# Kernel tuning notes

Measured on AMD Instinct MI355X. Metric: run time of the kernel, lower is better.

## Reference

```python
import jax, jax.numpy as jnp
import numpy as np

D_MODEL = 2048
N_HEADS = 16
N_KV = 4
D_HEAD = 128
D1 = 64
D2 = 64
WSIZE = 1024
EPS = 1e-6
ROPE_BASE = 10000.0


def _rmsnorm(x):
    # RMSNorm over last dim, no affine weight
    return x * jax.lax.rsqrt(jnp.mean(x * x, axis=-1, keepdims=True) + EPS)


def _apply_rope(x, cos, sin):
    # x: (..., D2); cos/sin: (1, T, 1, D2//2)
    h = D2 // 2
    x1, x2 = x[..., :h], x[..., h:]
    return jnp.concatenate([x1 * cos + x2 * sin, -x1 * sin + x2 * cos], axis=-1)


def setup_inputs() -> dict:
    key = jax.random.key(0)
    ks = jax.random.split(key, 6)
    B, T = 2, 2048
    return {
        "hidden_states": jax.random.normal(ks[0], (B, T, D_MODEL), dtype=jnp.float32),
        "W_qkv": jax.random.normal(ks[1], (D_MODEL, (N_HEADS + N_KV) * D_HEAD), dtype=jnp.float32) * 0.02,
        "W_rk": jax.random.normal(ks[2], (D_MODEL, D2), dtype=jnp.float32) * 0.02,
        "b_rk": jax.random.normal(ks[3], (D2,), dtype=jnp.float32) * 0.02,
        "softmax_scaler": jnp.ones((N_HEADS,), dtype=jnp.float32),
        "W_g": jax.random.normal(ks[5], (D_MODEL, D_MODEL), dtype=jnp.float32) * 0.02,
    }


def reference(hidden_states, W_qkv, W_rk, b_rk, softmax_scaler, W_g):
    x = hidden_states
    B, T, _ = x.shape
    # fused qkv projection + per-(head,token) RMSNorm (qk_norm)
    qkv = (x @ W_qkv).reshape(B, T, N_HEADS + N_KV, D_HEAD)
    qkv = _rmsnorm(qkv)
    q, kv = qkv[:, :, :N_HEADS], qkv[:, :, N_HEADS:]
    q_nope, q_rope = q[..., :D1], q[..., D1:]

    # head-tied rope key: shared across all heads
    k_rope = (x @ W_rk + b_rk)[:, :, None, :]  # (B, T, 1, D2)

    # rotary embedding (start_pos = 0)
    inv_freq = 1.0 / (ROPE_BASE ** (jnp.arange(0, D2, 2, dtype=jnp.float32) / D2))
    freqs = jnp.arange(T, dtype=jnp.float32)[:, None] * inv_freq[None, :]  # (T, D2//2)
    cos = jnp.cos(freqs)[None, :, None, :]
    sin = jnp.sin(freqs)[None, :, None, :]
    q_rope = _apply_rope(q_rope, cos, sin)
    k_rope = jnp.broadcast_to(_apply_rope(k_rope, cos, sin), (B, T, N_HEADS, D2))

    q = jnp.concatenate([q_nope, q_rope], axis=-1)  # (B, T, H, D_HEAD)

    # scalable softmax: scale q by per-head scaler * log(min(pos, wsize))
    pos = jnp.arange(1, T + 1, dtype=jnp.float32)
    log_pos = jnp.log(jnp.minimum(pos, float(WSIZE)))[None, :, None, None]
    q = softmax_scaler[None, None, :, None] * log_pos * q

    # tied k/v: first D1 of kv shared between k and v; repeat kv heads (GQA)
    kv_tied, v = kv[..., :D1], kv[..., D1:]
    rep = N_HEADS // N_KV
    kv_tied = jnp.repeat(kv_tied, rep, axis=2)  # (B, T, H, D1)
    v = jnp.repeat(v, rep, axis=2)              # (B, T, H, D2)
    k = jnp.concatenate([kv_tied, k_rope], axis=-1)   # (B, T, H, D_HEAD)
    v_full = jnp.concatenate([kv_tied, v], axis=-1)   # (B, T, H, D_HEAD)

    # sliding-window causal attention: key j valid iff i - WSIZE <= j <= i
    scores = jnp.einsum('bthd,bshd->bhts', q, k) / np.float32(np.sqrt(D_HEAD))
    i = jnp.arange(T)[:, None]
    j = jnp.arange(T)[None, :]
    mask = (j <= i) & (j >= i - WSIZE)
    scores = jnp.where(mask[None, None], scores, jnp.float32(-1e30))
    p = jax.nn.softmax(scores, axis=-1)
    y = jnp.einsum('bhts,bshd->bthd', p, v_full)  # (B, T, H, D_HEAD)

    # elementwise silu gate
    g = (x @ W_g).reshape(B, T, N_HEADS, D_HEAD)
    return y * jax.nn.silu(g)
```

## Files before the change

kernel.cpp:

```cpp
#include <hip/hip_runtime.h>

typedef _Float16 f16;
typedef _Float16 half8 __attribute__((ext_vector_type(8)));
typedef _Float16 half4_t __attribute__((ext_vector_type(4)));
typedef float f32x4 __attribute__((ext_vector_type(4)));

#define T_SEQ 2048
#define B_SZ 2
#define DM 2048
#define NH 16
#define NKV 4
#define DH 128
#define NQKV 2560
#define NALL 4736
#define NALLP 4864
#define COL_RK 2560
#define COL_G 2688
#define M_ROWS 4096
#define WIN 1024

typedef __attribute__((address_space(1))) const unsigned int guint;
typedef __attribute__((address_space(3))) unsigned int luint;
__device__ __forceinline__ void gload16(const void* g, void* l) {
  __builtin_amdgcn_global_load_lds((guint*)g, (luint*)l, 16, 0, 0);
}

__global__ void k_cvt(const float* __restrict__ in, f16* __restrict__ out, int n) {
  int i = (blockIdx.x * 256 + threadIdx.x) * 4;
  if (i >= n) return;
  float4 v = *(const float4*)(in + i);
  half4_t o;
  o[0] = (f16)v.x; o[1] = (f16)v.y; o[2] = (f16)v.z; o[3] = (f16)v.w;
  *(half4_t*)(out + i) = o;
}

__global__ __launch_bounds__(256) void k_cvt_t(const float* __restrict__ W,
                                               f16* __restrict__ Wt, int K, int N) {
  __shared__ float tile[32][33];
  int k0 = blockIdx.x * 32, n0 = blockIdx.y * 32;
  int tx = threadIdx.x & 31, ty = threadIdx.x >> 5;
#pragma unroll
  for (int r = 0; r < 32; r += 8)
    tile[ty + r][tx] = W[(size_t)(k0 + ty + r) * N + n0 + tx];
  __syncthreads();
#pragma unroll
  for (int r = 0; r < 32; r += 8)
    Wt[(size_t)(n0 + ty + r) * K + k0 + tx] = (f16)tile[tx][ty + r];
}

__global__ __launch_bounds__(256) void k_vt(const f16* __restrict__ v, f16* __restrict__ vt) {
  __shared__ f16 tile[32][34];
  int t0 = blockIdx.x * 32, d0 = blockIdx.y * 32, m = blockIdx.z;
  int tx = threadIdx.x & 31, ty = threadIdx.x >> 5;
  const f16* src = v + (size_t)m * T_SEQ * DH;
  f16* dst = vt + (size_t)m * T_SEQ * DH;
#pragma unroll
  for (int r = 0; r < 32; r += 8)
    tile[ty + r][tx] = src[(size_t)(t0 + ty + r) * DH + d0 + tx];
  __syncthreads();
#pragma unroll
  for (int r = 0; r < 32; r += 8)
    dst[(size_t)(d0 + ty + r) * T_SEQ + t0 + tx] = tile[tx][ty + r];
}

#define GEMM_PHASE(cb, kk, sb, koff)                                                        \
  {                                                                                         \
    char* Ab = lds + (cb) * 32768 + (kk) * 16384;                                           \
    char* Bb = lds + 65536 + (cb) * 16384 + (kk) * 8192;                                    \
    half8 af[4], bf[4];                                                                     \
    _Pragma("unroll")                                                                       \
    for (int i = 0; i < 4; ++i)                                                             \
      af[i] = *(const half8*)(Ab + (wm * 64 + i * 16 + fr) * 64 + xsl);                     \
    _Pragma("unroll")                                                                       \
    for (int j = 0; j < 4; ++j)                                                             \
      bf[j] = *(const half8*)(Bb + (wn * 64 + j * 16 + fr) * 64 + xsl);                     \
    gload16(Ag0 + (koff) + (kk) * 32, lds + (sb) * 32768 + (kk) * 16384 + w * 1024);        \
    gload16(Ag1 + (koff) + (kk) * 32, lds + (sb) * 32768 + (kk) * 16384 + 8192 + w * 1024); \
    gload16(Bg + (koff) + (kk) * 32, lds + 65536 + (sb) * 16384 + (kk) * 8192 + w * 1024);  \
    __builtin_amdgcn_s_barrier();                                                           \
    __builtin_amdgcn_sched_barrier(0);                                                      \
    asm volatile("s_waitcnt lgkmcnt(0)" ::: "memory");                                      \
    __builtin_amdgcn_sched_barrier(0);                                                      \
    __builtin_amdgcn_s_setprio(1);                                                          \
    _Pragma("unroll")                                                                       \
    for (int i = 0; i < 4; ++i)                                                             \
      _Pragma("unroll")                                                                     \
      for (int j = 0; j < 4; ++j)                                                           \
        acc[i][j] = __builtin_amdgcn_mfma_f32_16x16x32_f16(af[i], bf[j], acc[i][j], 0, 0, 0); \
    __builtin_amdgcn_s_setprio(0);                                                          \
    asm volatile("s_waitcnt vmcnt(3)" ::: "memory");                                        \
    __builtin_amdgcn_s_barrier();                                                           \
    __builtin_amdgcn_sched_barrier(0);                                                      \
  }

__global__ __launch_bounds__(512, 2) void k_gemm8(const f16* __restrict__ A,
                                                  const f16* __restrict__ Bt,
                                                  f16* __restrict__ C) {
  __shared__ __align__(16) char lds[98304];
  const int K = DM;
  unsigned orig = blockIdx.y * 38u + blockIdx.x;
  unsigned swz = (orig & 7u) * 76u + (orig >> 3);
  int m0 = (int)(swz / 38u) * 256;
  int n0 = (int)(swz % 38u) * 128;
  int tid = threadIdx.x, lane = tid & 63, w = tid >> 6;
  int wm = w >> 1, wn = w & 1;
  int fr = lane & 15, fq = lane >> 4;
  int xsl = (fq ^ ((fr >> 1) & 3)) << 4;
  int sr = tid >> 2, ss = tid & 3;
  int scol = (ss ^ ((sr >> 1) & 3)) * 8;
  f32x4 acc[4][4] = {};
  const f16* Ag0 = A + (size_t)(m0 + sr) * K + scol;
  const f16* Ag1 = A + (size_t)(m0 + 128 + sr) * K + scol;
  const f16* Bg  = Bt + (size_t)(n0 + sr) * K + scol;

  gload16(Ag0, lds + w * 1024);
  gload16(Ag1, lds + 8192 + w * 1024);
  gload16(Bg, lds + 65536 + w * 1024);
  gload16(Ag0 + 32, lds + 16384 + w * 1024);
  gload16(Ag1 + 32, lds + 16384 + 8192 + w * 1024);
  gload16(Bg + 32, lds + 65536 + 8192 + w * 1024);
  asm volatile("s_waitcnt vmcnt(3)" ::: "memory");
  __builtin_amdgcn_s_barrier();
  __builtin_amdgcn_sched_barrier(0);

  for (int kt = 0; kt < 32; ++kt) {
    int cb = kt & 1;
    int nt = kt < 31 ? kt + 1 : 31;
    int sb = nt & 1;
    int koff = nt * 64;
    GEMM_PHASE(cb, 0, sb, koff);
    GEMM_PHASE(cb, 1, sb, koff);
  }

#pragma unroll
  for (int i = 0; i < 4; ++i) {
    int row = m0 + wm * 64 + i * 16 + fq * 4;
#pragma unroll
    for (int j = 0; j < 4; ++j) {
      int col = n0 + wn * 64 + j * 16 + fr;
      f16* Cp = C + (size_t)row * NALLP + col;
#pragma unroll
      for (int rr = 0; rr < 4; ++rr) Cp[(size_t)rr * NALLP] = (f16)acc[i][j][rr];
    }
  }
}

__global__ __launch_bounds__(256) void k_postproc(
    const f16* __restrict__ CA,
    const float* __restrict__ brk, const float* __restrict__ sscal,
    f16* __restrict__ q16, f16* __restrict__ k16, f16* __restrict__ v16) {
  int row = blockIdx.x;
  int b = row >> 11, t = row & 2047;
  int lane = threadIdx.x & 63, wid = threadIdx.x >> 6;
  int ridx = lane & 31;
  float inv_freq = powf(10000.0f, -(float)(2 * ridx) / 64.0f);
  float fr = (float)t * inv_freq;
  float cs = cosf(fr), sn = sinf(fr);
  float logpos = logf(fminf((float)(t + 1), 1024.0f));
  const float rsqrt_d_log2e = 0.08838834764831845f * 1.4426950408889634f;
  const f16* Crow = CA + (size_t)row * NALLP;
#pragma unroll
  for (int p = 0; p < 5; ++p) {
    int h = p * 4 + wid;
    float v0 = (float)Crow[h * 128 + lane];
    float v1 = (float)Crow[h * 128 + 64 + lane];
    float ss = v0 * v0 + v1 * v1;
#pragma unroll
    for (int m = 1; m < 64; m <<= 1) ss += __shfl_xor(ss, m);
    float rms = rsqrtf(ss * (1.0f / 128.0f) + 1e-6f);
    v0 *= rms; v1 *= rms;
    if (h < NH) {
      float part = __shfl_xor(v1, 32);
      float vr = (lane < 32) ? (v1 * cs + part * sn) : (v1 * cs - part * sn);
      float scale = sscal[h] * logpos * rsqrt_d_log2e;
      size_t qb = ((size_t)(b * NH + h) * T_SEQ + t) * DH;
      q16[qb + lane]      = (f16)(v0 * scale);
      q16[qb + 64 + lane] = (f16)(vr * scale);
    } else {
      int hk = h - NH;
      size_t kb = ((size_t)(b * NKV + hk) * T_SEQ + t) * DH;
      k16[kb + lane]      = (f16)v0;
      v16[kb + lane]      = (f16)v0;
      v16[kb + 64 + lane] = (f16)v1;
    }
  }
  if (wid == 0) {
    float kr = (float)Crow[COL_RK + lane] + brk[lane];
    float part = __shfl_xor(kr, 32);
    float vr = (lane < 32) ? (kr * cs + part * sn) : (kr * cs - part * sn);
    f16 hv = (f16)vr;
#pragma unroll
    for (int hk = 0; hk < NKV; ++hk)
      k16[((size_t)(b * NKV + hk) * T_SEQ + t) * DH + 64 + lane] = hv;
  }
}

__global__ __launch_bounds__(512, 2) void k_attn(
    const f16* __restrict__ q16, const f16* __restrict__ k16, const f16* __restrict__ vt16,
    const f16* __restrict__ gA, float* __restrict__ out) {
  __shared__ __align__(16) f16 Ks[64 * DH];
  __shared__ __align__(16) f16 Vs[DH * 64];
  __shared__ __align__(16) f16 Ps[8 * 16 * 64];
  int bx = blockIdx.x;
  int qt = (bx & 1) ? (15 - (bx >> 1)) : (bx >> 1);
  int h = blockIdx.y, b = blockIdx.z, hk = h >> 2;
  int tid = threadIdx.x, lane = tid & 63, w = tid >> 6;
  int i0 = qt * 128, iw = i0 + w * 16;
  int fr = lane & 15, fq = lane >> 4;

  char* Ksb = (char*)Ks;
  char* Vsb = (char*)Vs;
  char* Psb = (char*)Ps + w * 2048;

  const f16* qbase = q16 + ((size_t)(b * NH + h) * T_SEQ + iw + fr) * DH;
  half8 qf[4];
#pragma unroll
  for (int kb = 0; kb < 4; ++kb) qf[kb] = *(const half8*)&qbase[kb * 32 + fq * 8];

  f32x4 o[8] = {};
  float mrow[4] = {-1e30f, -1e30f, -1e30f, -1e30f};
  float lrow[4] = {0.f, 0.f, 0.f, 0.f};

  const f16* kg = k16 + (size_t)(b * NKV + hk) * T_SEQ * DH;
  const f16* vg = vt16 + (size_t)(b * NKV + hk) * T_SEQ * DH;

  int jtTop = qt * 2 + 1;
  int jt0 = qt >= 8 ? qt * 2 - 16 : 0;
  for (int jt = jt0; jt <= jtTop; ++jt) {
    int j0 = jt * 64;
#pragma unroll
    for (int i = 0; i < 2; ++i) {
      int r = i * 32 + (tid >> 4);
      int c = (tid & 15) ^ (r & 7);
      gload16(kg + (size_t)(j0 + r) * DH + c * 8, Ksb + i * 8192 + w * 1024);
    }
#pragma unroll
    for (int i = 0; i < 2; ++i) {
      int r = i * 64 + (tid >> 3);
      int c = (tid & 7) ^ (r & 7);
      gload16(vg + (size_t)r * T_SEQ + j0 + c * 8, Vsb + i * 8192 + w * 1024);
    }
    __syncthreads();

    bool active = (jt == jtTop) ? (w >= 4)
                : ((qt >= 8 && jt == jt0) ? (w < 4) : true);
    if (active) {
      f32x4 s[4] = {};
      __builtin_amdgcn_s_setprio(1);
#pragma unroll
      for (int nf = 0; nf < 4; ++nf) {
        int row = nf * 16 + fr;
        int sw = fr & 7;
#pragma unroll
        for (int kb = 0; kb < 4; ++kb) {
          half8 bfv = *(const half8*)(Ksb + row * 256 + ((((kb << 2) | fq) ^ sw) << 4));
          s[nf] = __builtin_amdgcn_mfma_f32_16x16x32_f16(qf[kb], bfv, s[nf], 0, 0, 0);
        }
      }
      __builtin_amdgcn_s_setprio(0);
      int il = (w << 4) + (fq << 2);
      if (jt >= (qt << 1)) {
        int dc = (jt << 6) - i0;
#pragma unroll
        for (int nf = 0; nf < 4; ++nf) {
          int jo = nf * 16 + fr + dc;
#pragma unroll
          for (int r = 0; r < 4; ++r)
            if (jo > il + r) s[nf][r] = -3e38f;
        }
      } else if (qt >= 8 && jt - jt0 < 2) {
        int dl = (jt - jt0) << 6;
#pragma unroll
        for (int nf = 0; nf < 4; ++nf) {
          int jo = nf * 16 + fr + dl;
#pragma unroll
          for (int r = 0; r < 4; ++r)
            if (jo < il + r) s[nf][r] = -3e38f;
        }
      }
      float tm[4];
#pragma unroll
      for (int r = 0; r < 4; ++r)
        tm[r] = fmaxf(fmaxf(s[0][r], s[1][r]), fmaxf(s[2][r], s[3][r]));
#pragma unroll
      for (int r = 0; r < 4; ++r) {
        tm[r] = fmaxf(tm[r], __shfl_xor(tm[r], 1));
        tm[r] = fmaxf(tm[r], __shfl_xor(tm[r], 2));
        tm[r] = fmaxf(tm[r], __shfl_xor(tm[r], 4));
        tm[r] = fmaxf(tm[r], __shfl_xor(tm[r], 8));
      }
      bool need = false;
#pragma unroll
      for (int r = 0; r < 4; ++r) need = need || (tm[r] > mrow[r] + 8.0f);
      if (__any(need)) {
#pragma unroll
        for (int r = 0; r < 4; ++r) {
          float mn = fmaxf(mrow[r], tm[r]);
          float sc = exp2f(mrow[r] - mn);
          mrow[r] = mn;
          lrow[r] *= sc;
#pragma unroll
          for (int of = 0; of < 8; ++of) o[of][r] *= sc;
        }
      }
      float ls[4] = {0.f, 0.f, 0.f, 0.f};
#pragma unroll
      for (int nf = 0; nf < 4; ++nf)
#pragma unroll
        for (int r = 0; r < 4; ++r) {
          float pv = exp2f(s[nf][r] - mrow[r]);
          s[nf][r] = pv;
          ls[r] += pv;
        }
#pragma unroll
      for (int r = 0; r < 4; ++r) {
        float t2 = ls[r];
        t2 += __shfl_xor(t2, 1); t2 += __shfl_xor(t2, 2);
        t2 += __shfl_xor(t2, 4); t2 += __shfl_xor(t2, 8);
        lrow[r] += t2;
      }
#pragma unroll
      for (int nf = 0; nf < 4; ++nf) {
        int sbase = (nf << 1) + (fr >> 3);
        int boff = (fr & 7) << 1;
#pragma unroll
        for (int r = 0; r < 4; ++r) {
          int q = (fq << 2) + r;
          *(f16*)(Psb + q * 128 + ((sbase ^ (q & 7)) << 4) + boff) = (f16)s[nf][r];
        }
      }
      asm volatile("s_waitcnt lgkmcnt(0)" ::: "memory");
      __builtin_amdgcn_sched_barrier(0);
      half8 pf0 = *(const half8*)(Psb + fr * 128 + (((fq) ^ (fr & 7)) << 4));
      half8 pf1 = *(const half8*)(Psb + fr * 128 + (((4 | fq) ^ (fr & 7)) << 4));
      __builtin_amdgcn_s_setprio(1);
#pragma unroll
      for (int of = 0; of < 8; ++of) {
        int vrow0 = of * 16 + fr;
        int sw = fr & 7;
        half8 v0 = *(const half8*)(Vsb + vrow0 * 128 + ((fq ^ sw) << 4));
        half8 v1 = *(const half8*)(Vsb + vrow0 * 128 + (((4 | fq) ^ sw) << 4));
        o[of] = __builtin_amdgcn_mfma_f32_16x16x32_f16(pf0, v0, o[of], 0, 0, 0);
        o[of] = __builtin_amdgcn_mfma_f32_16x16x32_f16(pf1, v1, o[of], 0, 0, 0);
      }
      __builtin_amdgcn_s_setprio(0);
    }
    __syncthreads();
  }
  const f16* gb = gA + ((size_t)(b * T_SEQ) + iw) * NALLP + COL_G + h * DH;
  float* ob = out + ((size_t)(b * T_SEQ) + iw) * DM + h * DH;
#pragma unroll
  for (int r = 0; r < 4; ++r) {
    float inv = 1.0f / lrow[r];
    int ir = fq * 4 + r;
#pragma unroll
    for (int of = 0; of < 8; ++of) {
      int d = of * 16 + fr;
      float gv = (float)gb[(size_t)ir * NALLP + d];
      float sig = gv / (1.0f + expf(-gv));
      ob[(size_t)ir * DM + d] = o[of][r] * inv * sig;
    }
  }
}

extern "C" void kernel_launch(void* const* d_in, const int* in_sizes, int n_in,
                              void* d_out, int out_size, void* d_ws, size_t ws_size,
                              hipStream_t stream) {
  const float* x     = (const float*)d_in[0];
  const float* Wqkv  = (const float*)d_in[1];
  const float* Wrk   = (const float*)d_in[2];
  const float* brk   = (const float*)d_in[3];
  const float* sscal = (const float*)d_in[4];
  const float* Wg    = (const float*)d_in[5];
  float* out = (float*)d_out;
  char* ws = (char*)d_ws;
  size_t off = 0;
  auto alloc = [&](size_t bytes) -> void* {
    void* p = ws + off;
    off += (bytes + 255) & ~(size_t)255;
    return p;
  };
  f16* x16     = (f16*)alloc((size_t)M_ROWS * DM * 2);
  f16* BtAll   = (f16*)alloc((size_t)NALLP * DM * 2);
  f16* CAll    = (f16*)alloc((size_t)M_ROWS * NALLP * 2);
  f16* q16     = (f16*)alloc((size_t)B_SZ * NH * T_SEQ * DH * 2);
  f16* k16     = (f16*)alloc((size_t)B_SZ * NKV * T_SEQ * DH * 2);
  f16* v16     = (f16*)alloc((size_t)B_SZ * NKV * T_SEQ * DH * 2);
  f16* vt16    = (f16*)alloc((size_t)B_SZ * NKV * T_SEQ * DH * 2);

  k_cvt<<<(M_ROWS * DM / 4 + 255) / 256, 256, 0, stream>>>(x, x16, M_ROWS * DM);
  k_cvt_t<<<dim3(DM / 32, NQKV / 32), 256, 0, stream>>>(Wqkv, BtAll, DM, NQKV);
  k_cvt_t<<<dim3(DM / 32, 64 / 32), 256, 0, stream>>>(Wrk, BtAll + (size_t)COL_RK * DM, DM, 64);
  k_cvt_t<<<dim3(DM / 32, DM / 32), 256, 0, stream>>>(Wg, BtAll + (size_t)COL_G * DM, DM, DM);

  k_gemm8<<<dim3(NALLP / 128, M_ROWS / 256), 512, 0, stream>>>(x16, BtAll, CAll);

  k_postproc<<<M_ROWS, 256, 0, stream>>>(CAll, brk, sscal, q16, k16, v16);
  k_vt<<<dim3(T_SEQ / 32, DH / 32, B_SZ * NKV), 256, 0, stream>>>(v16, vt16);

  k_attn<<<dim3(T_SEQ / 128, NH, B_SZ), 512, 0, stream>>>(q16, k16, vt16, CAll, out);
}
```

Before: 360.0 us.

## Double-buffer K/V tiles in attention kernel to overlap loads with compute

Replaces the single K/V shared-memory tiles with two buffers in one 80 KB LDS array. The next key tile is prefetched with async global-to-LDS loads while the current tile is processed, so the load latency is hidden behind the MFMA work. LDS per block grows from 40 KB to 80 KB, which with launch_bounds(512,2) may stop two blocks from fitting per CU and reduce occupancy.

```diff
diff --git a/kernel.cpp b/kernel.cpp
--- a/kernel.cpp
+++ b/kernel.cpp
@@ -198,9 +198,7 @@
 __global__ __launch_bounds__(512, 2) void k_attn(
     const f16* __restrict__ q16, const f16* __restrict__ k16, const f16* __restrict__ vt16,
     const f16* __restrict__ gA, float* __restrict__ out) {
-  __shared__ __align__(16) f16 Ks[64 * DH];
-  __shared__ __align__(16) f16 Vs[DH * 64];
-  __shared__ __align__(16) f16 Ps[8 * 16 * 64];
+  __shared__ __align__(16) char lds[81920];
   int bx = blockIdx.x;
   int qt = (bx & 1) ? (15 - (bx >> 1)) : (bx >> 1);
   int h = blockIdx.y, b = blockIdx.z, hk = h >> 2;
@@ -208,9 +206,7 @@
   int i0 = qt * 128, iw = i0 + w * 16;
   int fr = lane & 15, fq = lane >> 4;
 
-  char* Ksb = (char*)Ks;
-  char* Vsb = (char*)Vs;
-  char* Psb = (char*)Ps + w * 2048;
+  char* Psb = lds + 65536 + w * 2048;
 
   const f16* qbase = q16 + ((size_t)(b * NH + h) * T_SEQ + iw + fr) * DH;
   half8 qf[4];
@@ -226,21 +222,30 @@
 
   int jtTop = qt * 2 + 1;
   int jt0 = qt >= 8 ? qt * 2 - 16 : 0;
+
+  int kr_ = tid >> 4, kc_ = ((tid & 15) ^ (kr_ & 7)) * 8;
+  int vr_ = tid >> 3, vc_ = ((tid & 7) ^ (vr_ & 7)) * 8;
+
+  auto STAGE = [&](int cbuf, int j0) {
+    char* Kb = lds + cbuf * 32768;
+    char* Vb = lds + cbuf * 32768 + 16384;
+#pragma unroll
+    for (int i = 0; i < 2; ++i)
+      gload16(kg + (size_t)(j0 + i * 32 + kr_) * DH + kc_, Kb + i * 8192 + w * 1024);
+#pragma unroll
+    for (int i = 0; i < 2; ++i)
+      gload16(vg + (size_t)(i * 64 + vr_) * T_SEQ + j0 + vc_, Vb + i * 8192 + w * 1024);
+  };
+
+  STAGE(0, jt0 * 64);
+  asm volatile("s_waitcnt vmcnt(0)" ::: "memory");
+  __syncthreads();
+  int cur = 0;
+
   for (int jt = jt0; jt <= jtTop; ++jt) {
-    int j0 = jt * 64;
-#pragma unroll
-    for (int i = 0; i < 2; ++i) {
-      int r = i * 32 + (tid >> 4);
-      int c = (tid & 15) ^ (r & 7);
-      gload16(kg + (size_t)(j0 + r) * DH + c * 8, Ksb + i * 8192 + w * 1024);
-    }
-#pragma unroll
-    for (int i = 0; i < 2; ++i) {
-      int r = i * 64 + (tid >> 3);
-      int c = (tid & 7) ^ (r & 7);
-      gload16(vg + (size_t)r * T_SEQ + j0 + c * 8, Vsb + i * 8192 + w * 1024);
-    }
-    __syncthreads();
+    if (jt < jtTop) STAGE(cur ^ 1, (jt + 1) * 64);
+    char* Ksb = lds + cur * 32768;
+    char* Vsb = lds + cur * 32768 + 16384;
 
     bool active = (jt == jtTop) ? (w >= 4)
                 : ((qt >= 8 && jt == jt0) ? (w < 4) : true);
@@ -345,7 +350,9 @@
       }
       __builtin_amdgcn_s_setprio(0);
     }
+    asm volatile("s_waitcnt vmcnt(0)" ::: "memory");
     __syncthreads();
+    cur ^= 1;
   }
   const f16* gb = gA + ((size_t)(b * T_SEQ) + iw) * NALLP + COL_G + h * DH;
   float* ob = out + ((size_t)(b * T_SEQ) + iw) * DM + h * DH;
```

After: 348.4 us. -3.2%, faster.
